# Kernel tuning notes

Hardware: AMD Instinct MI355X
Metric: run time of the kernel (lower is better)

Reference implementation:

```python
import jax, jax.numpy as jnp
import numpy as np

NUM_USERS = 60000
NUM_ITEMS = 40000
N_NODES = NUM_USERS + NUM_ITEMS
EMBED_K = 128
E_HALF = 1_000_000  # bipartite interactions; symmetrized -> 2M directed edges


def setup_inputs() -> dict:
    key = jax.random.key(0)
    k1, k2, k3, k4, k5, k6, k7 = jax.random.split(key, 7)
    scale = 1.0 / np.sqrt(EMBED_K)  # ~ xavier_normal
    Gu = jax.random.normal(k1, (NUM_USERS, EMBED_K), jnp.float32) * scale
    Gi = jax.random.normal(k2, (NUM_ITEMS, EMBED_K), jnp.float32) * scale
    W0 = jax.random.normal(k3, (EMBED_K, EMBED_K), jnp.float32) * scale
    W1 = jax.random.normal(k4, (EMBED_K, EMBED_K), jnp.float32) * scale
    W2 = jax.random.normal(k5, (EMBED_K, EMBED_K), jnp.float32) * scale
    # bipartite user-item graph, symmetrized (items offset by NUM_USERS)
    u = jax.random.randint(k6, (E_HALF,), 0, NUM_USERS)
    it = jax.random.randint(k7, (E_HALF,), 0, NUM_ITEMS) + NUM_USERS
    src = jnp.concatenate([u, it])
    dst = jnp.concatenate([it, u])
    edge_index = jnp.stack([src, dst]).astype(jnp.int32)  # [2, 2M]
    return {"Gu": Gu, "Gi": Gi, "W0": W0, "W1": W1, "W2": W2,
            "edge_index": edge_index}


def reference(Gu, Gi, W0, W1, W2, edge_index):
    # add_self_loops=False, bias=False) -> ReLU), then split into (gu, gi).
    src, dst = edge_index[0], edge_index[1]
    n_users = Gu.shape[0]
    n_nodes = Gu.shape[0] + Gi.shape[0]
    # PyG gcn_norm (no self loops): deg = scatter(1, col); norm = d^-1/2[row]*d^-1/2[col]
    ones = jnp.ones(src.shape, Gu.dtype)
    deg = jax.ops.segment_sum(ones, dst, num_segments=n_nodes)
    dinv = jnp.where(deg > 0, jax.lax.rsqrt(jnp.maximum(deg, 1.0)), 0.0)
    norm = dinv[src] * dinv[dst]  # [E]
    x = jnp.concatenate([Gu, Gi], axis=0)  # [N, d]
    for W in (W0, W1, W2):
        h = x @ W                                   # [N, d] dense GEMM
        msg = h[src] * norm[:, None]                # [E, d] gather + scale
        x = jax.nn.relu(jax.ops.segment_sum(msg, dst, num_segments=n_nodes))
    return x[:n_users], x[n_users:]
```

## Files before the change

### kernel.cpp

```cpp
#include <hip/hip_runtime.h>
#include <hip/hip_bf16.h>

#define EMB 128
#define NPB 256
#define NB_PAD 512
#define CHUNK 4096

typedef unsigned int uint32;
typedef __attribute__((ext_vector_type(8))) short bf16x8;
typedef __attribute__((ext_vector_type(4))) float f32x4;

__device__ __forceinline__ ushort f2bf(float f) {
    uint32 u = __float_as_uint(f);
    return (ushort)((u + 0x7fff + ((u >> 16) & 1)) >> 16);
}
__device__ __forceinline__ uint32 pack_hi2(uint32 u0, uint32 u1) {
    return (u1 & 0xffff0000u) | (u0 >> 16);
}


__global__ __launch_bounds__(256) void bucket_count_kernel(
    const int* __restrict__ dst, int* __restrict__ bucket_cnt, int E, int NB) {
    __shared__ int cnt[NB_PAD];
    int t = threadIdx.x;
    long e0 = (long)blockIdx.x * CHUNK;
    int n = E - (int)e0; if (n > CHUNK) n = CHUNK;
    for (int b = t; b < NB_PAD; b += 256) cnt[b] = 0;
    __syncthreads();
    #pragma unroll
    for (int i = 0; i < CHUNK / 256; i++) {
        int idx = t + i * 256;
        if (idx < n) atomicAdd(&cnt[dst[e0 + idx] >> 8], 1);
    }
    __syncthreads();
    for (int b = t; b < NB; b += 256)
        if (cnt[b] > 0) atomicAdd(&bucket_cnt[b], cnt[b]);
}

__global__ void bucket_scan_kernel(const int* __restrict__ bucket_cnt,
                                   int* __restrict__ ebase, int* __restrict__ gcursor,
                                   int NB, int E) {
    __shared__ int sc[512];
    int t = threadIdx.x;
    int v = (t < NB) ? bucket_cnt[t] : 0;
    sc[t] = v;
    __syncthreads();
    for (int off = 1; off < 512; off <<= 1) {
        int u = (t >= off) ? sc[t - off] : 0;
        __syncthreads();
        sc[t] += u;
        __syncthreads();
    }
    if (t < NB) {
        int excl = sc[t] - v;
        ebase[t] = excl;
        gcursor[t] = excl;
    }
    if (t == 0) ebase[NB] = E;
}


__global__ __launch_bounds__(256) void bucket_scatter_kernel(
    const int* __restrict__ src, const int* __restrict__ dst,
    int* __restrict__ gcursor, uint2* __restrict__ ebuf, int E, int NB) {
    __shared__ int cnt[NB_PAD];
    __shared__ int loff[NB_PAD];
    __shared__ int gbase[NB_PAD];
    __shared__ int pos[NB_PAD];
    __shared__ int sc[256];
    __shared__ uint2 stage[CHUNK];
    int t = threadIdx.x;
    long e0 = (long)blockIdx.x * CHUNK;
    int n = E - (int)e0; if (n > CHUNK) n = CHUNK;
    for (int b = t; b < NB_PAD; b += 256) { cnt[b] = 0; pos[b] = 0; }
    __syncthreads();
    int es[CHUNK / 256], ed[CHUNK / 256];
    #pragma unroll
    for (int i = 0; i < CHUNK / 256; i++) {
        int idx = t + i * 256;
        if (idx < n) {
            es[i] = src[e0 + idx];
            ed[i] = dst[e0 + idx];
            atomicAdd(&cnt[ed[i] >> 8], 1);
        }
    }
    __syncthreads();
    int a = cnt[2 * t], b2 = cnt[2 * t + 1];
    sc[t] = a + b2;
    __syncthreads();
    for (int off = 1; off < 256; off <<= 1) {
        int v = (t >= off) ? sc[t - off] : 0;
        __syncthreads();
        sc[t] += v;
        __syncthreads();
    }
    int excl = sc[t] - (a + b2);
    loff[2 * t] = excl;
    loff[2 * t + 1] = excl + a;
    __syncthreads();
    for (int b = t; b < NB; b += 256)
        if (cnt[b] > 0) gbase[b] = atomicAdd(&gcursor[b], cnt[b]);
    __syncthreads();
    #pragma unroll
    for (int i = 0; i < CHUNK / 256; i++) {
        int idx = t + i * 256;
        if (idx < n) {
            int b = ed[i] >> 8;
            int p = atomicAdd(&pos[b], 1);
            stage[loff[b] + p] = make_uint2((uint32)es[i], (uint32)ed[i]);
        }
    }
    __syncthreads();
    for (int b = t; b < NB; b += 256) {
        int c = cnt[b], lo = loff[b], go = gbase[b];
        for (int k = 0; k < c; k++) ebuf[go + k] = stage[lo + k];
    }
}


__global__ __launch_bounds__(256) void bucket_deg_kernel(
    const uint2* __restrict__ ebuf, const int* __restrict__ ebase,
    int* __restrict__ deg, float* __restrict__ dinv, int N) {
    __shared__ int cnt[NPB];
    int t = threadIdx.x;
    int n0 = blockIdx.x * NPB;
    int nn = N - n0; if (nn > NPB) nn = NPB;
    cnt[t] = 0;
    __syncthreads();
    int e0 = ebase[blockIdx.x];
    int e1 = ebase[blockIdx.x + 1];
    for (int e = e0 + t; e < e1; e += 256) {
        uint2 sd = ebuf[e];
        atomicAdd(&cnt[(int)sd.y - n0], 1);
    }
    __syncthreads();
    if (t < nn) {
        int c = cnt[t];
        deg[n0 + t] = c;
        dinv[n0 + t] = c > 0 ? rsqrtf((float)c) : 0.0f;
    }
}


__global__ void scan1_kernel(const int* __restrict__ deg, int* __restrict__ rowptr,
                             int* __restrict__ bsum, int N) {
    __shared__ int sc[256];
    int t = threadIdx.x;
    int base = blockIdx.x * 1024 + t * 4;
    int d0 = 0, d1 = 0, d2 = 0, d3 = 0;
    if (base + 3 < N) {
        int4 v = *(const int4*)(deg + base);
        d0 = v.x; d1 = v.y; d2 = v.z; d3 = v.w;
    } else {
        if (base     < N) d0 = deg[base];
        if (base + 1 < N) d1 = deg[base + 1];
        if (base + 2 < N) d2 = deg[base + 2];
        if (base + 3 < N) d3 = deg[base + 3];
    }
    int s = d0 + d1 + d2 + d3;
    sc[t] = s;
    __syncthreads();
    for (int off = 1; off < 256; off <<= 1) {
        int v = (t >= off) ? sc[t - off] : 0;
        __syncthreads();
        sc[t] += v;
        __syncthreads();
    }
    int excl = sc[t] - s;
    if (t == 255) bsum[blockIdx.x] = sc[255];
    int dd[4] = {d0, d1, d2, d3};
    int p = excl;
    #pragma unroll
    for (int j = 0; j < 4; j++) {
        int i = base + j;
        if (i < N) rowptr[i] = p;
        p += dd[j];
    }
}

__global__ void scan2_kernel(int* bsum, int nb) {
    __shared__ int sc[128];
    int t = threadIdx.x;
    int v = (t < nb) ? bsum[t] : 0;
    sc[t] = v;
    __syncthreads();
    for (int off = 1; off < 128; off <<= 1) {
        int u = (t >= off) ? sc[t - off] : 0;
        __syncthreads();
        sc[t] += u;
        __syncthreads();
    }
    if (t < nb) bsum[t] = sc[t] - v;
}

__global__ void scan3_kernel(int* __restrict__ rowptr, const int* __restrict__ bsum,
                             int N, int E) {
    int t = threadIdx.x, b = blockIdx.x;
    int add = bsum[b];
    int base = b * 1024 + t * 4;
    #pragma unroll
    for (int j = 0; j < 4; j++) {
        int i = base + j;
        if (i < N) rowptr[i] += add;
    }
    if (b == 0 && t == 0) rowptr[N] = E;
}


__global__ __launch_bounds__(256) void bucket_fill_kernel(
    const uint2* __restrict__ ebuf, const int* __restrict__ rowptr,
    int* __restrict__ csr, int N) {
    __shared__ int cnt[NPB];
    __shared__ int rp[NPB];
    int t = threadIdx.x;
    int n0 = blockIdx.x * NPB;
    int nn = N - n0; if (nn > NPB) nn = NPB;
    if (t < nn) { cnt[t] = 0; rp[t] = rowptr[n0 + t]; }
    __syncthreads();
    int e0 = rowptr[n0];
    int e1 = rowptr[n0 + nn];
    for (int e = e0 + t; e < e1; e += 256) {
        uint2 sd = ebuf[e];
        int local = (int)sd.y - n0;
        int p = atomicAdd(&cnt[local], 1);
        csr[rp[local] + p] = (int)sd.x;
    }
}


__global__ __launch_bounds__(256) void agg_relu_kernel(
    const uint32* __restrict__ Yh,
    const int* __restrict__ rowptr, const int* __restrict__ csr,
    const float* __restrict__ dinv, float* __restrict__ out, int N) {
    int node = blockIdx.x * 4 + (threadIdx.x >> 6);
    int lane = threadIdx.x & 63;
    if (node >= N) return;
    int e0 = rowptr[node], e1 = rowptr[node + 1];
    float ax = 0.0f, ay = 0.0f;
    for (int base = e0; base < e1; base += 64) {
        int n = e1 - base;
        if (n > 64) n = 64;
        int s = 0;
        float w = 0.0f;
        if (lane < n) {
            s = csr[base + lane];
            w = dinv[s];
        }
        int nn = (n + 15) & ~15;
        for (int j = 0; j < nn; j += 16) {
            uint32 p[16];
            float wj[16];
            #pragma unroll
            for (int u = 0; u < 16; u++) {
                int sj = __shfl(s, j + u);
                wj[u] = __shfl(w, j + u);
                p[u] = Yh[(size_t)sj * 64 + lane];
            }
            #pragma unroll
            for (int u = 0; u < 16; u++) {
                ax += wj[u] * __uint_as_float(p[u] << 16);
                ay += wj[u] * __uint_as_float(p[u] & 0xffff0000u);
            }
        }
    }
    float wd = dinv[node];
    float2 r;
    r.x = fmaxf(ax * wd, 0.0f);
    r.y = fmaxf(ay * wd, 0.0f);
    *(float2*)(out + (size_t)node * EMB + lane * 2) = r;
}


__global__ void wsplit_kernel(const float* __restrict__ W0, const float* __restrict__ W1,
                              const float* __restrict__ W2,
                              ushort* __restrict__ Whi, ushort* __restrict__ Wlo) {
    const float* W = (blockIdx.x == 0) ? W0 : (blockIdx.x == 1) ? W1 : W2;
    ushort* hiT = Whi + blockIdx.x * EMB * EMB;
    ushort* loT = Wlo + blockIdx.x * EMB * EMB;
    for (int i = threadIdx.x; i < EMB * EMB; i += blockDim.x) {
        int k = i >> 7, n = i & 127;
        float w = W[i];
        uint32 u = __float_as_uint(w);
        ushort hi = (ushort)(u >> 16);
        float hif = __uint_as_float(u & 0xffff0000u);
        ushort lo = f2bf(w - hif);
        hiT[n * EMB + k] = hi;
        loT[n * EMB + k] = lo;
    }
}


union FragU { uint32 u[4]; bf16x8 v; };

__global__ __launch_bounds__(256, 2) void gemm_mfma_kernel(
    const float* __restrict__ A, const ushort* __restrict__ WhiT,
    const ushort* __restrict__ WloT, ushort* __restrict__ Yh, int M) {
    __shared__ float As[16][132];
    int t = threadIdx.x;
    int wv = t >> 6, lane = t & 63, quad = lane >> 4, l16 = lane & 15;

    FragU bfr[8][2];
    #pragma unroll
    for (int kc = 0; kc < 8; kc++) {
        const ushort* srcW = (kc < 4) ? WhiT : WloT;
        int kb = (kc & 3) * 32 + quad * 8;
        #pragma unroll
        for (int c = 0; c < 2; c++) {
            int n = wv * 32 + c * 16 + l16;
            const uint32* p = (const uint32*)(srcW + n * EMB + kb);
            bfr[kc][c].u[0] = p[0];
            bfr[kc][c].u[1] = p[1];
            bfr[kc][c].u[2] = p[2];
            bfr[kc][c].u[3] = p[3];
        }
    }

    int srow = t >> 4, skq = t & 15;
    int ntile = (M + 15) >> 4;
    for (int tile = blockIdx.x; tile < ntile; tile += (int)gridDim.x) {
        int r0 = tile << 4;
        __syncthreads();
        {
            float4 v0 = {0.f, 0.f, 0.f, 0.f}, v1 = v0;
            int row = r0 + srow;
            if (row < M) {
                const float* ga = A + (size_t)row * EMB + skq * 8;
                v0 = *(const float4*)ga;
                v1 = *(const float4*)(ga + 4);
            }
            *(float4*)&As[srow][skq * 8] = v0;
            *(float4*)&As[srow][skq * 8 + 4] = v1;
        }
        __syncthreads();

        FragU ah[4], al[4];
        #pragma unroll
        for (int kc = 0; kc < 4; kc++) {
            const float* p = &As[l16][kc * 32 + quad * 8];
            float4 xa = *(const float4*)p;
            float4 xb = *(const float4*)(p + 4);
            uint32 u0 = __float_as_uint(xa.x), u1 = __float_as_uint(xa.y);
            uint32 u2 = __float_as_uint(xa.z), u3 = __float_as_uint(xa.w);
            uint32 u4 = __float_as_uint(xb.x), u5 = __float_as_uint(xb.y);
            uint32 u6 = __float_as_uint(xb.z), u7 = __float_as_uint(xb.w);
            ah[kc].u[0] = pack_hi2(u0, u1);
            ah[kc].u[1] = pack_hi2(u2, u3);
            ah[kc].u[2] = pack_hi2(u4, u5);
            ah[kc].u[3] = pack_hi2(u6, u7);
            float l0 = xa.x - __uint_as_float(u0 & 0xffff0000u);
            float l1 = xa.y - __uint_as_float(u1 & 0xffff0000u);
            float l2 = xa.z - __uint_as_float(u2 & 0xffff0000u);
            float l3 = xa.w - __uint_as_float(u3 & 0xffff0000u);
            float l4 = xb.x - __uint_as_float(u4 & 0xffff0000u);
            float l5 = xb.y - __uint_as_float(u5 & 0xffff0000u);
            float l6 = xb.z - __uint_as_float(u6 & 0xffff0000u);
            float l7 = xb.w - __uint_as_float(u7 & 0xffff0000u);
            al[kc].u[0] = pack_hi2(__float_as_uint(l0), __float_as_uint(l1));
            al[kc].u[1] = pack_hi2(__float_as_uint(l2), __float_as_uint(l3));
            al[kc].u[2] = pack_hi2(__float_as_uint(l4), __float_as_uint(l5));
            al[kc].u[3] = pack_hi2(__float_as_uint(l6), __float_as_uint(l7));
        }

        f32x4 acc0 = {0.f, 0.f, 0.f, 0.f};
        f32x4 acc1 = {0.f, 0.f, 0.f, 0.f};
        #pragma unroll
        for (int kc = 0; kc < 4; kc++) {
            acc0 = __builtin_amdgcn_mfma_f32_16x16x32_bf16(ah[kc].v, bfr[kc][0].v, acc0, 0, 0, 0);
            acc1 = __builtin_amdgcn_mfma_f32_16x16x32_bf16(ah[kc].v, bfr[kc][1].v, acc1, 0, 0, 0);
        }
        #pragma unroll
        for (int kc = 0; kc < 4; kc++) {
            acc0 = __builtin_amdgcn_mfma_f32_16x16x32_bf16(ah[kc].v, bfr[kc + 4][0].v, acc0, 0, 0, 0);
            acc1 = __builtin_amdgcn_mfma_f32_16x16x32_bf16(ah[kc].v, bfr[kc + 4][1].v, acc1, 0, 0, 0);
        }
        #pragma unroll
        for (int kc = 0; kc < 4; kc++) {
            acc0 = __builtin_amdgcn_mfma_f32_16x16x32_bf16(al[kc].v, bfr[kc][0].v, acc0, 0, 0, 0);
            acc1 = __builtin_amdgcn_mfma_f32_16x16x32_bf16(al[kc].v, bfr[kc][1].v, acc1, 0, 0, 0);
        }

        int colb = wv * 32 + l16;
        #pragma unroll
        for (int r = 0; r < 4; r++) {
            int row = r0 + quad * 4 + r;
            if (row < M) {
                Yh[(size_t)row * EMB + colb]      = f2bf(acc0[r]);
                Yh[(size_t)row * EMB + colb + 16] = f2bf(acc1[r]);
            }
        }
    }
}


extern "C" void kernel_launch(void* const* d_in, const int* in_sizes, int n_in,
                              void* d_out, int out_size, void* d_ws, size_t ws_size,
                              hipStream_t stream) {
    (void)n_in; (void)out_size; (void)ws_size;
    const float* Gu = (const float*)d_in[0];
    const float* Gi = (const float*)d_in[1];
    const float* W0 = (const float*)d_in[2];
    const float* W1 = (const float*)d_in[3];
    const float* W2 = (const float*)d_in[4];
    const int* ei = (const int*)d_in[5];

    int nu = in_sizes[0] / EMB;
    int ni = in_sizes[1] / EMB;
    int N = nu + ni;
    int E = in_sizes[5] / 2;
    const int* src = ei;
    const int* dst = ei + E;
    int NB = (N + NPB - 1) / NPB;

    ushort* Yh      = (ushort*)d_ws;
    uint2* ebuf     = (uint2*)(Yh + (size_t)N * EMB);
    int* deg        = (int*)(ebuf + (size_t)E);
    int* rowptr     = deg + N;
    float* dinv     = (float*)(rowptr + N + 1);
    int* csr        = (int*)(dinv + N);
    int* bucket_cnt = csr + E;
    int* ebase      = bucket_cnt + NB;
    int* gcursor    = ebase + NB + 1;
    int* bsum       = gcursor + NB;
    ushort* WhiT    = (ushort*)(bsum + 128);
    ushort* WloT    = WhiT + 3 * EMB * EMB;
    float* X        = (float*)d_out;

    hipMemsetAsync(bucket_cnt, 0, sizeof(int) * (size_t)NB, stream);

    wsplit_kernel<<<3, 256, 0, stream>>>(W0, W1, W2, WhiT, WloT);

    int ecb = (E + CHUNK - 1) / CHUNK;
    bucket_count_kernel<<<ecb, 256, 0, stream>>>(dst, bucket_cnt, E, NB);
    bucket_scan_kernel<<<1, 512, 0, stream>>>(bucket_cnt, ebase, gcursor, NB, E);
    bucket_scatter_kernel<<<ecb, 256, 0, stream>>>(src, dst, gcursor, ebuf, E, NB);
    bucket_deg_kernel<<<NB, 256, 0, stream>>>(ebuf, ebase, deg, dinv, N);
    int nb = (N + 1023) / 1024;
    scan1_kernel<<<nb, 256, 0, stream>>>(deg, rowptr, bsum, N);
    scan2_kernel<<<1, 128, 0, stream>>>(bsum, nb);
    scan3_kernel<<<nb, 256, 0, stream>>>(rowptr, bsum, N, E);
    bucket_fill_kernel<<<NB, 256, 0, stream>>>(ebuf, rowptr, csr, N);

    int aggBlocks = (N + 3) / 4;
    const int GB = 512;

    gemm_mfma_kernel<<<GB, 256, 0, stream>>>(Gu, WhiT, WloT, Yh, nu);
    gemm_mfma_kernel<<<GB, 256, 0, stream>>>(Gi, WhiT, WloT, Yh + (size_t)nu * EMB, ni);
    agg_relu_kernel<<<aggBlocks, 256, 0, stream>>>((const uint32*)Yh, rowptr, csr, dinv, X, N);
    gemm_mfma_kernel<<<GB, 256, 0, stream>>>(X, WhiT + EMB * EMB, WloT + EMB * EMB, Yh, N);
    agg_relu_kernel<<<aggBlocks, 256, 0, stream>>>((const uint32*)Yh, rowptr, csr, dinv, X, N);
    gemm_mfma_kernel<<<GB, 256, 0, stream>>>(X, WhiT + 2 * EMB * EMB, WloT + 2 * EMB * EMB, Yh, N);
    agg_relu_kernel<<<aggBlocks, 256, 0, stream>>>((const uint32*)Yh, rowptr, csr, dinv, X, N);
}
```

Measured before the change: 470.5 us.

## Store GEMM output in column panels, prescale by dinv, panel-parallel aggregation

The GEMM now writes its bf16 output in eight 16-column panels (panel-major layout) and folds the source-side dinv scaling into the epilogue, so the aggregation no longer loads a per-edge weight. Aggregation launches one block per (32-node group, panel), with 8 lanes per node each reading one uint32 (2 bf16) of a 32-byte panel row, unrolled by 4 edges. The aim is for each panel (~3.2MB) to stay resident in cache while it is gathered. The GEMM also drops the LDS staging and loads A fragments straight from global memory, drops the occupancy hint and uses a doubled grid. The cost is 32-byte scattered gathers instead of 256-byte rows, and divergence within a wave when node degrees differ.

Result: slower. 688.4 us (+46.3%).

```diff
diff --git a/kernel.cpp b/kernel.cpp
--- a/kernel.cpp
+++ b/kernel.cpp
@@ -228,46 +228,37 @@
 }
 
 
-__global__ __launch_bounds__(256) void agg_relu_kernel(
-    const uint32* __restrict__ Yh,
+__global__ __launch_bounds__(256) void agg_panel_kernel(
+    const uint32* __restrict__ Yhp,
     const int* __restrict__ rowptr, const int* __restrict__ csr,
     const float* __restrict__ dinv, float* __restrict__ out, int N) {
-    int node = blockIdx.x * 4 + (threadIdx.x >> 6);
-    int lane = threadIdx.x & 63;
-    if (node >= N) return;
-    int e0 = rowptr[node], e1 = rowptr[node + 1];
+    int panel = blockIdx.x & 7;
+    int wv = threadIdx.x >> 6, lane = threadIdx.x & 63;
+    int ns = lane >> 3, d = lane & 7;
+    int node = (blockIdx.x >> 3) * 32 + wv * 8 + ns;
+    const uint32* pD = Yhp + (size_t)panel * N * 8;
     float ax = 0.0f, ay = 0.0f;
-    for (int base = e0; base < e1; base += 64) {
-        int n = e1 - base;
-        if (n > 64) n = 64;
-        int s = 0;
-        float w = 0.0f;
-        if (lane < n) {
-            s = csr[base + lane];
-            w = dinv[s];
-        }
-        int nn = (n + 15) & ~15;
-        for (int j = 0; j < nn; j += 16) {
-            uint32 p[16];
-            float wj[16];
-            #pragma unroll
-            for (int u = 0; u < 16; u++) {
-                int sj = __shfl(s, j + u);
-                wj[u] = __shfl(w, j + u);
-                p[u] = Yh[(size_t)sj * 64 + lane];
-            }
-            #pragma unroll
-            for (int u = 0; u < 16; u++) {
-                ax += wj[u] * __uint_as_float(p[u] << 16);
-                ay += wj[u] * __uint_as_float(p[u] & 0xffff0000u);
-            }
-        }
-    }
-    float wd = dinv[node];
-    float2 r;
-    r.x = fmaxf(ax * wd, 0.0f);
-    r.y = fmaxf(ay * wd, 0.0f);
-    *(float2*)(out + (size_t)node * EMB + lane * 2) = r;
+    int e = 0, ee = 0;
+    if (node < N) { e = rowptr[node]; ee = rowptr[node + 1]; }
+    while (__any(e < ee)) {
+        uint32 p0 = 0, p1 = 0, p2 = 0, p3 = 0;
+        if (e < ee)     p0 = pD[(size_t)csr[e] * 8 + d];
+        if (e + 1 < ee) p1 = pD[(size_t)csr[e + 1] * 8 + d];
+        if (e + 2 < ee) p2 = pD[(size_t)csr[e + 2] * 8 + d];
+        if (e + 3 < ee) p3 = pD[(size_t)csr[e + 3] * 8 + d];
+        ax += __uint_as_float(p0 << 16) + __uint_as_float(p1 << 16)
+            + __uint_as_float(p2 << 16) + __uint_as_float(p3 << 16);
+        ay += __uint_as_float(p0 & 0xffff0000u) + __uint_as_float(p1 & 0xffff0000u)
+            + __uint_as_float(p2 & 0xffff0000u) + __uint_as_float(p3 & 0xffff0000u);
+        e += 4;
+    }
+    if (node < N) {
+        float wd = dinv[node];
+        float2 r;
+        r.x = fmaxf(ax * wd, 0.0f);
+        r.y = fmaxf(ay * wd, 0.0f);
+        *(float2*)(out + (size_t)node * EMB + panel * 16 + d * 2) = r;
+    }
 }
 
 
@@ -292,10 +283,10 @@
 
 union FragU { uint32 u[4]; bf16x8 v; };
 
-__global__ __launch_bounds__(256, 2) void gemm_mfma_kernel(
+__global__ __launch_bounds__(256) void gemm_mfma_kernel(
     const float* __restrict__ A, const ushort* __restrict__ WhiT,
-    const ushort* __restrict__ WloT, ushort* __restrict__ Yh, int M) {
-    __shared__ float As[16][132];
+    const ushort* __restrict__ WloT, const float* __restrict__ dinv,
+    ushort* __restrict__ Yhp, int M, int rowOff, int Ntot) {
     int t = threadIdx.x;
     int wv = t >> 6, lane = t & 63, quad = lane >> 4, l16 = lane & 15;
 
@@ -315,77 +306,67 @@
         }
     }
 
-    int srow = t >> 4, skq = t & 15;
     int ntile = (M + 15) >> 4;
     for (int tile = blockIdx.x; tile < ntile; tile += (int)gridDim.x) {
         int r0 = tile << 4;
-        __syncthreads();
-        {
-            float4 v0 = {0.f, 0.f, 0.f, 0.f}, v1 = v0;
-            int row = r0 + srow;
-            if (row < M) {
-                const float* ga = A + (size_t)row * EMB + skq * 8;
-                v0 = *(const float4*)ga;
-                v1 = *(const float4*)(ga + 4);
-            }
-            *(float4*)&As[srow][skq * 8] = v0;
-            *(float4*)&As[srow][skq * 8 + 4] = v1;
-        }
-        __syncthreads();
-
-        FragU ah[4], al[4];
+        int arow = r0 + l16;
+        bool rv = arow < M;
+        const float* ap = A + (size_t)(rv ? arow : 0) * EMB + quad * 8;
+
+        float4 xa[4], xb[4];
         #pragma unroll
         for (int kc = 0; kc < 4; kc++) {
-            const float* p = &As[l16][kc * 32 + quad * 8];
-            float4 xa = *(const float4*)p;
-            float4 xb = *(const float4*)(p + 4);
-            uint32 u0 = __float_as_uint(xa.x), u1 = __float_as_uint(xa.y);
-            uint32 u2 = __float_as_uint(xa.z), u3 = __float_as_uint(xa.w);
-            uint32 u4 = __float_as_uint(xb.x), u5 = __float_as_uint(xb.y);
-            uint32 u6 = __float_as_uint(xb.z), u7 = __float_as_uint(xb.w);
-            ah[kc].u[0] = pack_hi2(u0, u1);
-            ah[kc].u[1] = pack_hi2(u2, u3);
-            ah[kc].u[2] = pack_hi2(u4, u5);
-            ah[kc].u[3] = pack_hi2(u6, u7);
-            float l0 = xa.x - __uint_as_float(u0 & 0xffff0000u);
-            float l1 = xa.y - __uint_as_float(u1 & 0xffff0000u);
-            float l2 = xa.z - __uint_as_float(u2 & 0xffff0000u);
-            float l3 = xa.w - __uint_as_float(u3 & 0xffff0000u);
-            float l4 = xb.x - __uint_as_float(u4 & 0xffff0000u);
-            float l5 = xb.y - __uint_as_float(u5 & 0xffff0000u);
-            float l6 = xb.z - __uint_as_float(u6 & 0xffff0000u);
-            float l7 = xb.w - __uint_as_float(u7 & 0xffff0000u);
-            al[kc].u[0] = pack_hi2(__float_as_uint(l0), __float_as_uint(l1));
-            al[kc].u[1] = pack_hi2(__float_as_uint(l2), __float_as_uint(l3));
-            al[kc].u[2] = pack_hi2(__float_as_uint(l4), __float_as_uint(l5));
-            al[kc].u[3] = pack_hi2(__float_as_uint(l6), __float_as_uint(l7));
+            if (rv) {
+                xa[kc] = *(const float4*)(ap + kc * 32);
+                xb[kc] = *(const float4*)(ap + kc * 32 + 4);
+            } else {
+                xa[kc] = (float4){0.f, 0.f, 0.f, 0.f};
+                xb[kc] = xa[kc];
+            }
         }
 
         f32x4 acc0 = {0.f, 0.f, 0.f, 0.f};
         f32x4 acc1 = {0.f, 0.f, 0.f, 0.f};
         #pragma unroll
         for (int kc = 0; kc < 4; kc++) {
-            acc0 = __builtin_amdgcn_mfma_f32_16x16x32_bf16(ah[kc].v, bfr[kc][0].v, acc0, 0, 0, 0);
-            acc1 = __builtin_amdgcn_mfma_f32_16x16x32_bf16(ah[kc].v, bfr[kc][1].v, acc1, 0, 0, 0);
-        }
-        #pragma unroll
-        for (int kc = 0; kc < 4; kc++) {
-            acc0 = __builtin_amdgcn_mfma_f32_16x16x32_bf16(ah[kc].v, bfr[kc + 4][0].v, acc0, 0, 0, 0);
-            acc1 = __builtin_amdgcn_mfma_f32_16x16x32_bf16(ah[kc].v, bfr[kc + 4][1].v, acc1, 0, 0, 0);
-        }
-        #pragma unroll
-        for (int kc = 0; kc < 4; kc++) {
-            acc0 = __builtin_amdgcn_mfma_f32_16x16x32_bf16(al[kc].v, bfr[kc][0].v, acc0, 0, 0, 0);
-            acc1 = __builtin_amdgcn_mfma_f32_16x16x32_bf16(al[kc].v, bfr[kc][1].v, acc1, 0, 0, 0);
-        }
-
-        int colb = wv * 32 + l16;
+            uint32 u0 = __float_as_uint(xa[kc].x), u1 = __float_as_uint(xa[kc].y);
+            uint32 u2 = __float_as_uint(xa[kc].z), u3 = __float_as_uint(xa[kc].w);
+            uint32 u4 = __float_as_uint(xb[kc].x), u5 = __float_as_uint(xb[kc].y);
+            uint32 u6 = __float_as_uint(xb[kc].z), u7 = __float_as_uint(xb[kc].w);
+            FragU ah, al;
+            ah.u[0] = pack_hi2(u0, u1);
+            ah.u[1] = pack_hi2(u2, u3);
+            ah.u[2] = pack_hi2(u4, u5);
+            ah.u[3] = pack_hi2(u6, u7);
+            float l0 = xa[kc].x - __uint_as_float(u0 & 0xffff0000u);
+            float l1 = xa[kc].y - __uint_as_float(u1 & 0xffff0000u);
+            float l2 = xa[kc].z - __uint_as_float(u2 & 0xffff0000u);
+            float l3 = xa[kc].w - __uint_as_float(u3 & 0xffff0000u);
+            float l4 = xb[kc].x - __uint_as_float(u4 & 0xffff0000u);
+            float l5 = xb[kc].y - __uint_as_float(u5 & 0xffff0000u);
+            float l6 = xb[kc].z - __uint_as_float(u6 & 0xffff0000u);
+            float l7 = xb[kc].w - __uint_as_float(u7 & 0xffff0000u);
+            al.u[0] = pack_hi2(__float_as_uint(l0), __float_as_uint(l1));
+            al.u[1] = pack_hi2(__float_as_uint(l2), __float_as_uint(l3));
+            al.u[2] = pack_hi2(__float_as_uint(l4), __float_as_uint(l5));
+            al.u[3] = pack_hi2(__float_as_uint(l6), __float_as_uint(l7));
+            acc0 = __builtin_amdgcn_mfma_f32_16x16x32_bf16(ah.v, bfr[kc][0].v, acc0, 0, 0, 0);
+            acc1 = __builtin_amdgcn_mfma_f32_16x16x32_bf16(ah.v, bfr[kc][1].v, acc1, 0, 0, 0);
+            acc0 = __builtin_amdgcn_mfma_f32_16x16x32_bf16(ah.v, bfr[kc + 4][0].v, acc0, 0, 0, 0);
+            acc1 = __builtin_amdgcn_mfma_f32_16x16x32_bf16(ah.v, bfr[kc + 4][1].v, acc1, 0, 0, 0);
+            acc0 = __builtin_amdgcn_mfma_f32_16x16x32_bf16(al.v, bfr[kc][0].v, acc0, 0, 0, 0);
+            acc1 = __builtin_amdgcn_mfma_f32_16x16x32_bf16(al.v, bfr[kc][1].v, acc1, 0, 0, 0);
+        }
+
         #pragma unroll
         for (int r = 0; r < 4; r++) {
-            int row = r0 + quad * 4 + r;
-            if (row < M) {
-                Yh[(size_t)row * EMB + colb]      = f2bf(acc0[r]);
-                Yh[(size_t)row * EMB + colb + 16] = f2bf(acc1[r]);
+            int rr = r0 + quad * 4 + r;
+            if (rr < M) {
+                float wd = dinv[rowOff + rr];
+                size_t i0 = ((size_t)(2 * wv) * Ntot + rowOff + rr) * 16 + l16;
+                size_t i1 = ((size_t)(2 * wv + 1) * Ntot + rowOff + rr) * 16 + l16;
+                Yhp[i0] = f2bf(acc0[r] * wd);
+                Yhp[i1] = f2bf(acc1[r] * wd);
             }
         }
     }
@@ -411,8 +392,8 @@
     const int* dst = ei + E;
     int NB = (N + NPB - 1) / NPB;
 
-    ushort* Yh      = (ushort*)d_ws;
-    uint2* ebuf     = (uint2*)(Yh + (size_t)N * EMB);
+    ushort* Yhp     = (ushort*)d_ws;
+    uint2* ebuf     = (uint2*)(Yhp + (size_t)N * EMB);
     int* deg        = (int*)(ebuf + (size_t)E);
     int* rowptr     = deg + N;
     float* dinv     = (float*)(rowptr + N + 1);
@@ -440,14 +421,14 @@
     scan3_kernel<<<nb, 256, 0, stream>>>(rowptr, bsum, N, E);
     bucket_fill_kernel<<<NB, 256, 0, stream>>>(ebuf, rowptr, csr, N);
 
-    int aggBlocks = (N + 3) / 4;
-    const int GB = 512;
-
-    gemm_mfma_kernel<<<GB, 256, 0, stream>>>(Gu, WhiT, WloT, Yh, nu);
-    gemm_mfma_kernel<<<GB, 256, 0, stream>>>(Gi, WhiT, WloT, Yh + (size_t)nu * EMB, ni);
-    agg_relu_kernel<<<aggBlocks, 256, 0, stream>>>((const uint32*)Yh, rowptr, csr, dinv, X, N);
-    gemm_mfma_kernel<<<GB, 256, 0, stream>>>(X, WhiT + EMB * EMB, WloT + EMB * EMB, Yh, N);
-    agg_relu_kernel<<<aggBlocks, 256, 0, stream>>>((const uint32*)Yh, rowptr, csr, dinv, X, N);
-    gemm_mfma_kernel<<<GB, 256, 0, stream>>>(X, WhiT + 2 * EMB * EMB, WloT + 2 * EMB * EMB, Yh, N);
-    agg_relu_kernel<<<aggBlocks, 256, 0, stream>>>((const uint32*)Yh, rowptr, csr, dinv, X, N);
-}
+    int aggBlocks = ((N + 31) / 32) * 8;
+    const int GB = 1024;
+
+    gemm_mfma_kernel<<<GB, 256, 0, stream>>>(Gu, WhiT, WloT, dinv, Yhp, nu, 0, N);
+    gemm_mfma_kernel<<<GB, 256, 0, stream>>>(Gi, WhiT, WloT, dinv, Yhp, ni, nu, N);
+    agg_panel_kernel<<<aggBlocks, 256, 0, stream>>>((const uint32*)Yhp, rowptr, csr, dinv, X, N);
+    gemm_mfma_kernel<<<GB, 256, 0, stream>>>(X, WhiT + EMB * EMB, WloT + EMB * EMB, dinv, Yhp, N, 0, N);
+    agg_panel_kernel<<<aggBlocks, 256, 0, stream>>>((const uint32*)Yhp, rowptr, csr, dinv, X, N);
+    gemm_mfma_kernel<<<GB, 256, 0, stream>>>(X, WhiT + 2 * EMB * EMB, WloT + 2 * EMB * EMB, dinv, Yhp, N, 0, N);
+    agg_panel_kernel<<<aggBlocks, 256, 0, stream>>>((const uint32*)Yhp, rowptr, csr, dinv, X, N);
+}
```
